# Kernel optimization log

Hardware: AMD Instinct MI355X
Metric: run time of the kernel (lower is better)

The kernel has to match this reference:

```python
import jax, jax.numpy as jnp
import numpy as np

D_MODEL = 1024
N_HEADS = 16
D_K = D_MODEL // N_HEADS
ROPE_THETA = 10000.0


def setup_inputs() -> dict:
    key = jax.random.key(0)
    ks = jax.random.split(key, 5)
    B, S = 2, 2048
    std = (2.0 / (D_MODEL + D_MODEL)) ** 0.5
    x = jax.random.normal(ks[0], (B, S, D_MODEL), dtype=jnp.float32)
    Wq = jax.random.normal(ks[1], (D_MODEL, D_MODEL), dtype=jnp.float32) * std
    Wk = jax.random.normal(ks[2], (D_MODEL, D_MODEL), dtype=jnp.float32) * std
    Wv = jax.random.normal(ks[3], (D_MODEL, D_MODEL), dtype=jnp.float32) * std
    Wo = jax.random.normal(ks[4], (D_MODEL, D_MODEL), dtype=jnp.float32) * std
    token_positions = jnp.arange(S, dtype=jnp.int64 if jax.config.jax_enable_x64 else jnp.int32)
    return {"x": x, "Wq": Wq, "Wk": Wk, "Wv": Wv, "Wo": Wo,
            "token_positions": token_positions}


def _apply_rope(t, token_positions):
    # t: [B, H, S, d_k]; token_positions: [S]
    inv_freq = 1.0 / (ROPE_THETA ** (jnp.arange(0, D_K, 2, dtype=jnp.float32) / D_K))  # [d_k/2]
    freqs = token_positions.astype(jnp.float32)[:, None] * inv_freq[None, :]  # [S, d_k/2]
    cos, sin = jnp.cos(freqs), jnp.sin(freqs)
    x1, x2 = t[..., ::2], t[..., 1::2]
    xr = x1 * cos - x2 * sin
    yr = x1 * sin + x2 * cos
    # interleave back to even/odd positions
    out = jnp.stack([xr, yr], axis=-1).reshape(t.shape)
    return out


def reference(x, Wq, Wk, Wv, Wo, token_positions):
    B, S, D = x.shape
    H, dk = N_HEADS, D_K
    # projections: weight is [d_out, d_in], applied as x @ W.T
    def proj_heads(W):
        y = jnp.einsum('bsd,ed->bse', x, W)
        return y.reshape(B, S, H, dk).transpose(0, 2, 1, 3)  # [B,H,S,dk]
    q = proj_heads(Wq)
    k = proj_heads(Wk)
    v = proj_heads(Wv)
    q = _apply_rope(q, token_positions)
    k = _apply_rope(k, token_positions)
    scores = jnp.einsum('bhqd,bhkd->bhqk', q, k) / jnp.sqrt(jnp.float32(dk))
    causal = jnp.tril(jnp.ones((S, S), dtype=bool))
    scores = jnp.where(causal, scores, -jnp.inf)
    attn = jax.nn.softmax(scores, axis=-1)
    out = jnp.einsum('bhqk,bhkd->bhqd', attn, v)  # [B,H,S,dk]
    out = out.transpose(0, 2, 1, 3).reshape(B, S, D)
    return jnp.einsum('bsd,ed->bse', out, Wo)
```

## Files before the change

### kernel.cpp

```cpp
#include <hip/hip_runtime.h>

typedef __bf16 bf16x8 __attribute__((ext_vector_type(8)));
typedef float f32x4 __attribute__((ext_vector_type(4)));
typedef unsigned short u16x8 __attribute__((ext_vector_type(8)));


__device__ __forceinline__ unsigned short f2bf(float f) {
  unsigned u = __builtin_bit_cast(unsigned, f);
  u = (u + 0x7FFFu + ((u >> 16) & 1u)) >> 16;
  return (unsigned short)u;
}

__device__ __forceinline__ unsigned cvt_pk_bf16(float lo, float hi) {
  unsigned r;
  asm("v_cvt_pk_bf16_f32 %0, %1, %2" : "=v"(r) : "v"(lo), "v"(hi));
  return r;
}

__device__ __forceinline__ void load_lds16(const void* g, void* l) {
  __builtin_amdgcn_global_load_lds(
      (__attribute__((address_space(1))) void*)g,
      (__attribute__((address_space(3))) void*)l, 16, 0, 0);
}

__global__ __launch_bounds__(256) void k_convert(
    const float* __restrict__ x,
    const float* __restrict__ wq, const float* __restrict__ wk,
    const float* __restrict__ wv, const float* __restrict__ wo,
    unsigned short* __restrict__ xb,
    unsigned short* __restrict__ wqb, unsigned short* __restrict__ wkb,
    unsigned short* __restrict__ wvb, unsigned short* __restrict__ wob) {
  const int g = blockIdx.x * 256 + threadIdx.x;
  const float* src;
  unsigned short* dst;
  int off;
  if (g < (1 << 20)) {
    src = x; dst = xb; off = g;
  } else {
    const int q = g - (1 << 20);
    const int t = q >> 18;
    off = q & ((1 << 18) - 1);
    src = (t == 0) ? wq : (t == 1) ? wk : (t == 2) ? wv : wo;
    dst = (t == 0) ? wqb : (t == 1) ? wkb : (t == 2) ? wvb : wob;
  }
  const float4 v = ((const float4*)src)[off];
  ushort4 r;
  r.x = f2bf(v.x); r.y = f2bf(v.y); r.z = f2bf(v.z); r.w = f2bf(v.w);
  ((ushort4*)dst)[off] = r;
}

__global__ __launch_bounds__(256) void k_rope_tab(const int* __restrict__ tpos,
                                                  float* __restrict__ ct,
                                                  float* __restrict__ st) {
  const int idx = blockIdx.x * 256 + threadIdx.x;
  const int s = idx >> 5, i = idx & 31;
  const double p = (double)tpos[s];
  const double f = p * pow(10000.0, -(double)(2 * i) / 64.0);
  ct[idx] = (float)cos(f);
  st[idx] = (float)sin(f);
}

__device__ __forceinline__ void gemm_core_1024(
    const unsigned short* __restrict__ Ag,
    const unsigned short* __restrict__ Bg,
    unsigned short* As, unsigned short* Bs, f32x4 (&acc)[4][4], int tid) {
  const int lane = tid & 63;
  const int w = tid >> 6;
  const int wm = (w >> 1) * 64;
  const int wn = (w & 1) * 64;
  const int lr = lane & 15;
  const int lg8 = (lane >> 4) * 8;
  const int c0 = tid, c1 = 256 + tid;
  const int ar0 = c0 >> 2, ac0 = (c0 & 3) * 8;
  const int ar1 = c1 >> 2, ac1 = (c1 & 3) * 8;

  auto stage = [&](int buf, int kt) {
    unsigned short* Ab = As + buf * 4096;
    unsigned short* Bb = Bs + buf * 4096;
    load_lds16(Ag + ar0 * 1024 + kt + ac0, Ab + c0 * 8);
    load_lds16(Ag + ar1 * 1024 + kt + ac1, Ab + c1 * 8);
    load_lds16(Bg + ar0 * 1024 + kt + ac0, Bb + c0 * 8);
    load_lds16(Bg + ar1 * 1024 + kt + ac1, Bb + c1 * 8);
  };

  stage(0, 0);
  stage(1, 32);
  int cur = 0;
  for (int ki = 0; ki < 32; ++ki) {
    if (ki + 2 < 32) {
      int nb = cur + 2; if (nb >= 3) nb -= 3;
      stage(nb, (ki + 2) * 32);
      asm volatile("s_waitcnt vmcnt(8)" ::: "memory");
    } else if (ki + 1 < 32) {
      asm volatile("s_waitcnt vmcnt(4)" ::: "memory");
    } else {
      asm volatile("s_waitcnt vmcnt(0)" ::: "memory");
    }
    __builtin_amdgcn_s_barrier();
    const unsigned short* Ab = As + cur * 4096;
    const unsigned short* Bb = Bs + cur * 4096;
    bf16x8 af[4], bfv[4];
#pragma unroll
    for (int mi = 0; mi < 4; ++mi)
      af[mi] = *(const bf16x8*)(Ab + (wm + mi * 16 + lr) * 32 + lg8);
#pragma unroll
    for (int ni = 0; ni < 4; ++ni)
      bfv[ni] = *(const bf16x8*)(Bb + (wn + ni * 16 + lr) * 32 + lg8);
    __builtin_amdgcn_s_setprio(1);
#pragma unroll
    for (int mi = 0; mi < 4; ++mi)
#pragma unroll
      for (int ni = 0; ni < 4; ++ni)
        acc[mi][ni] = __builtin_amdgcn_mfma_f32_16x16x32_bf16(
            af[mi], bfv[ni], acc[mi][ni], 0, 0, 0);
    __builtin_amdgcn_s_setprio(0);
    __builtin_amdgcn_s_barrier();
    ++cur; if (cur == 3) cur = 0;
  }
}

__global__ __launch_bounds__(256) void k_proj(
    const unsigned short* __restrict__ Xb,
    const unsigned short* __restrict__ Wq, const unsigned short* __restrict__ Wk,
    const unsigned short* __restrict__ Wv,
    const float* __restrict__ ctab, const float* __restrict__ stab,
    unsigned short* __restrict__ Qo, unsigned short* __restrict__ Ko,
    unsigned short* __restrict__ Vo) {
  __shared__ __align__(16) unsigned short As[3 * 128 * 32];
  __shared__ __align__(16) unsigned short Bs[3 * 128 * 32];
  const int z = blockIdx.z;
  const unsigned short* Wsel = (z == 0) ? Wq : (z == 1) ? Wk : Wv;
  unsigned short* Out = (z == 0) ? Qo : (z == 1) ? Ko : Vo;
  const int tid = threadIdx.x;
  const int bm = blockIdx.x * 128, bn = blockIdx.y * 128;
  f32x4 acc[4][4] = {};
  gemm_core_1024(Xb + (size_t)bm * 1024, Wsel + (size_t)bn * 1024, As, Bs, acc, tid);

  const int lane = tid & 63, w = tid >> 6;
  const int wm = (w >> 1) * 64, wn = (w & 1) * 64;
  const int lr = lane & 15, lg = lane >> 4;

  if (z == 2) {
#pragma unroll
    for (int mi = 0; mi < 4; ++mi) {
      const int r0 = bm + wm + mi * 16 + lg * 4;
      const int s = r0 & 2047, b = r0 >> 11;
#pragma unroll
      for (int ni = 0; ni < 4; ++ni) {
        const int e = bn + wn + ni * 16 + lr;
        const int h = e >> 6, d = e & 63;
        ushort4 pk;
        pk.x = f2bf(acc[mi][ni][0]);
        pk.y = f2bf(acc[mi][ni][1]);
        pk.z = f2bf(acc[mi][ni][2]);
        pk.w = f2bf(acc[mi][ni][3]);
        *(ushort4*)&Out[((size_t)(b * 16 + h) * 64 + d) * 2048 + s] = pk;
      }
    }
    return;
  }

  const bool odd = lane & 1;
#pragma unroll
  for (int mi = 0; mi < 4; ++mi) {
#pragma unroll
    for (int ni = 0; ni < 4; ++ni) {
#pragma unroll
      for (int reg = 0; reg < 4; ++reg) {
        const int r = bm + wm + mi * 16 + lg * 4 + reg;
        const int e = bn + wn + ni * 16 + lr;
        float val = acc[mi][ni][reg];
        const float partner = __shfl_xor(val, 1);
        const int s = r & 2047, b = r >> 11;
        const int h = e >> 6, d = e & 63;
        const int i = d >> 1;
        const float c = ctab[s * 32 + i];
        const float sn = stab[s * 32 + i];
        const float outv = odd ? (val * c + partner * sn) : (val * c - partner * sn);
        Out[((size_t)(b * 16 + h) * 2048 + s) * 64 + d] = f2bf(outv);
      }
    }
  }
}

__global__ __launch_bounds__(64, 2) void k_attn(
    const unsigned short* __restrict__ Q, const unsigned short* __restrict__ K,
    const unsigned short* __restrict__ Vt, unsigned short* __restrict__ O) {
  __shared__ __align__(16) unsigned short Vs[2][64 * 64];
  __shared__ __align__(16) unsigned short Pl[16 * 68];
  const int L = blockIdx.x;
  const int bh = (L & 7) * 4 + ((L >> 3) & 3);
  const int p = L >> 5;
  const int qrowA = p * 16, qrowB = (127 - p) * 16;
  const int Ta = (qrowA + 79) >> 6;
  const int Tb = (qrowB + 79) >> 6;
  const int TT = Ta + Tb;
  const int lane = threadIdx.x & 63;
  const int lr = lane & 15, lg = lane >> 4;
  const unsigned short* Qg = Q + (size_t)bh * 2048 * 64;
  const unsigned short* Kg = K + (size_t)bh * 2048 * 64;
  const unsigned short* Vg = Vt + (size_t)bh * 64 * 2048;

  bf16x8 qfA[2], qfB[2];
#pragma unroll
  for (int h = 0; h < 2; ++h) {
    qfA[h] = *(const bf16x8*)(Qg + (qrowA + lr) * 64 + h * 32 + lg * 8);
    qfB[h] = *(const bf16x8*)(Qg + (qrowB + lr) * 64 + h * 32 + lg * 8);
  }

  u16x8 ouv;
#pragma unroll
  for (int j = 0; j < 8; ++j) ouv[j] = 0x3F80;
  const bf16x8 onesf = __builtin_bit_cast(bf16x8, ouv);

  f32x4 oA[4] = {}, oB[4] = {};
  float mA[4], lA[4], mB[4], lB[4];
#pragma unroll
  for (int r = 0; r < 4; ++r) {
    mA[r] = -__builtin_inff(); lA[r] = 0.f;
    mB[r] = -__builtin_inff(); lB[r] = 0.f;
  }

  const float SCL = 0.125f * 1.44269504088896f;

  const int kbase = lr * 64 + lg * 8;
  const int vbase = (lane >> 3) * 2048 + (((lane & 7) ^ (lane >> 3)) * 8);

  auto kvof = [&](int t) { return (t < Tb) ? t : t - Tb; };
  auto loadK = [&](bf16x8 (&kd)[4][2], int kv) {
    const unsigned short* base = Kg + (size_t)kv * 4096 + kbase;
#pragma unroll
    for (int nt = 0; nt < 4; ++nt)
#pragma unroll
      for (int h = 0; h < 2; ++h)
        kd[nt][h] = *(const bf16x8*)(base + nt * 1024 + h * 32);
  };
  auto issueV = [&](int buf, int kv) {
    const unsigned short* src = Vg + kv * 64 + vbase;
    unsigned short* dst = &Vs[buf][0] + lane * 8;
#pragma unroll
    for (int i0 = 0; i0 < 8; ++i0)
      load_lds16(src + i0 * 16384, dst + i0 * 512);
  };

  auto core = [&](bf16x8 (&kc)[4][2], int kv, int T, bf16x8 (&qf)[2],
                  float (&m)[4], float (&l)[4], f32x4 (&oacc)[4], int qrow,
                  int vbuf, bool more) {
    const int kv0 = kv * 64;
    f32x4 sacc[4];
    __builtin_amdgcn_s_setprio(1);
#pragma unroll
    for (int nt = 0; nt < 4; ++nt) {
      f32x4 z = {0.f, 0.f, 0.f, 0.f};
      z = __builtin_amdgcn_mfma_f32_16x16x32_bf16(qf[0], kc[nt][0], z, 0, 0, 0);
      sacc[nt] = __builtin_amdgcn_mfma_f32_16x16x32_bf16(qf[1], kc[nt][1], z, 0, 0, 0);
    }
    __builtin_amdgcn_s_setprio(0);

    const bool needmask = (kv == T - 1);
    float pm[4];
#pragma unroll
    for (int r = 0; r < 4; ++r) pm[r] = -__builtin_inff();
#pragma unroll
    for (int nt = 0; nt < 4; ++nt)
#pragma unroll
      for (int reg = 0; reg < 4; ++reg) {
        float sv = sacc[nt][reg];
        if (needmask) {
          const int kg = kv0 + nt * 16 + lr;
          const int qg = qrow + lg * 4 + reg;
          if (kg > qg) sv = -__builtin_inff();
        }
        sacc[nt][reg] = sv;
        pm[reg] = fmaxf(pm[reg], sv);
      }
#pragma unroll
    for (int off = 1; off < 16; off <<= 1)
#pragma unroll
      for (int reg = 0; reg < 4; ++reg)
        pm[reg] = fmaxf(pm[reg], __shfl_xor(pm[reg], off));

    float gm = -1.f;
#pragma unroll
    for (int reg = 0; reg < 4; ++reg) gm = fmaxf(gm, pm[reg] - m[reg]);
    float msc[4];
    if (__any(gm > 0.f)) {
#pragma unroll
      for (int reg = 0; reg < 4; ++reg) {
        const float mn = fmaxf(m[reg], pm[reg]);
        const float al = exp2f(SCL * (m[reg] - mn));
        m[reg] = mn;
        msc[reg] = SCL * mn;
        l[reg] *= al;
#pragma unroll
        for (int nt = 0; nt < 4; ++nt) oacc[nt][reg] *= al;
      }
    } else {
#pragma unroll
      for (int reg = 0; reg < 4; ++reg) msc[reg] = SCL * m[reg];
    }

#pragma unroll
    for (int nt = 0; nt < 4; ++nt) {
      const float p0 = exp2f(sacc[nt][0] * SCL - msc[0]);
      const float p1 = exp2f(sacc[nt][1] * SCL - msc[1]);
      const float p2 = exp2f(sacc[nt][2] * SCL - msc[2]);
      const float p3 = exp2f(sacc[nt][3] * SCL - msc[3]);
      const unsigned w01 = cvt_pk_bf16(p0, p1);
      const unsigned w23 = cvt_pk_bf16(p2, p3);
      unsigned short* base = Pl + (lg * 4) * 68 + nt * 16 + lr;
      base[0] = (unsigned short)w01;
      base[68] = (unsigned short)(w01 >> 16);
      base[136] = (unsigned short)w23;
      base[204] = (unsigned short)(w23 >> 16);
    }
    bf16x8 pa[2];
#pragma unroll
    for (int ks = 0; ks < 2; ++ks)
      pa[ks] = *(const bf16x8*)(Pl + lr * 68 + ks * 32 + lg * 8);

    if (more) asm volatile("s_waitcnt vmcnt(16)" ::: "memory");
    else      asm volatile("s_waitcnt vmcnt(0)" ::: "memory");

    const unsigned short* Vw = &Vs[vbuf][0];
    __builtin_amdgcn_s_setprio(1);
    {
      f32x4 z = {0.f, 0.f, 0.f, 0.f};
      z = __builtin_amdgcn_mfma_f32_16x16x32_bf16(pa[0], onesf, z, 0, 0, 0);
      z = __builtin_amdgcn_mfma_f32_16x16x32_bf16(pa[1], onesf, z, 0, 0, 0);
#pragma unroll
      for (int reg = 0; reg < 4; ++reg) l[reg] += z[reg];
    }
#pragma unroll
    for (int nt = 0; nt < 4; ++nt) {
      const int row = nt * 16 + lr;
      const bf16x8 vb0 = *(const bf16x8*)(Vw + row * 64 + ((lg ^ (row & 7)) * 8));
      const bf16x8 vb1 = *(const bf16x8*)(Vw + row * 64 + (((lg + 4) ^ (row & 7)) * 8));
      oacc[nt] = __builtin_amdgcn_mfma_f32_16x16x32_bf16(pa[0], vb0, oacc[nt], 0, 0, 0);
      oacc[nt] = __builtin_amdgcn_mfma_f32_16x16x32_bf16(pa[1], vb1, oacc[nt], 0, 0, 0);
    }
    __builtin_amdgcn_s_setprio(0);
  };

  bf16x8 kbufA[4][2], kbufB[4][2];
  loadK(kbufA, 0);
  issueV(0, 0);

  auto iter = [&](int t, bf16x8 (&kc)[4][2], bf16x8 (&kn)[4][2]) {
    const int nxt = t + 1;
    const bool more = (nxt < TT);
    if (more) {
      const int kvn = kvof(nxt);
      loadK(kn, kvn);
      issueV(nxt & 1, kvn);
    }
    if (t < Tb) core(kc, t, Tb, qfB, mB, lB, oB, qrowB, t & 1, more);
    else        core(kc, t - Tb, Ta, qfA, mA, lA, oA, qrowA, t & 1, more);
  };

  int t = 0;
  for (;;) {
    iter(t, kbufA, kbufB); ++t; if (t >= TT) break;
    iter(t, kbufB, kbufA); ++t; if (t >= TT) break;
  }

  const int b = bh >> 4, h = bh & 15;
#pragma unroll
  for (int reg = 0; reg < 4; ++reg) {
    const float invA = 1.0f / lA[reg];
    const float invB = 1.0f / lB[reg];
    const int sA = qrowA + lg * 4 + reg;
    const int sB = qrowB + lg * 4 + reg;
#pragma unroll
    for (int nt = 0; nt < 4; ++nt) {
      const int dv = nt * 16 + lr;
      O[((size_t)b * 2048 + sA) * 1024 + h * 64 + dv] = f2bf(oA[nt][reg] * invA);
      O[((size_t)b * 2048 + sB) * 1024 + h * 64 + dv] = f2bf(oB[nt][reg] * invB);
    }
  }
}

__global__ __launch_bounds__(256) void k_out(const unsigned short* __restrict__ Ab,
                                             const unsigned short* __restrict__ Wo,
                                             float* __restrict__ Out) {
  __shared__ __align__(16) unsigned short As[3 * 128 * 32];
  __shared__ __align__(16) unsigned short Bs[3 * 128 * 32];
  const int tid = threadIdx.x;
  const int bm = blockIdx.x * 128, bn = blockIdx.y * 128;
  f32x4 acc[4][4] = {};
  gemm_core_1024(Ab + (size_t)bm * 1024, Wo + (size_t)bn * 1024, As, Bs, acc, tid);
  const int lane = tid & 63, w = tid >> 6;
  const int wm = (w >> 1) * 64, wn = (w & 1) * 64;
  const int lr = lane & 15, lg = lane >> 4;
#pragma unroll
  for (int mi = 0; mi < 4; ++mi)
#pragma unroll
    for (int ni = 0; ni < 4; ++ni)
#pragma unroll
      for (int reg = 0; reg < 4; ++reg) {
        const int r = bm + wm + mi * 16 + lg * 4 + reg;
        const int e = bn + wn + ni * 16 + lr;
        Out[(size_t)r * 1024 + e] = acc[mi][ni][reg];
      }
}

extern "C" void kernel_launch(void* const* d_in, const int* in_sizes, int n_in,
                              void* d_out, int out_size, void* d_ws, size_t ws_size,
                              hipStream_t stream) {
  const float* x = (const float*)d_in[0];
  const float* Wq = (const float*)d_in[1];
  const float* Wk = (const float*)d_in[2];
  const float* Wv = (const float*)d_in[3];
  const float* Wo = (const float*)d_in[4];
  const int* tpos = (const int*)d_in[5];
  float* out = (float*)d_out;
  char* ws = (char*)d_ws;
  const size_t MB = 1024 * 1024;
  unsigned short* xb = (unsigned short*)(ws);
  unsigned short* wqb = (unsigned short*)(ws + 8 * MB);
  unsigned short* wkb = (unsigned short*)(ws + 10 * MB);
  unsigned short* wvb = (unsigned short*)(ws + 12 * MB);
  unsigned short* wob = (unsigned short*)(ws + 14 * MB);
  unsigned short* Qb = (unsigned short*)(ws + 16 * MB);
  unsigned short* Kb = (unsigned short*)(ws + 24 * MB);
  unsigned short* Vtb = (unsigned short*)(ws + 32 * MB);
  unsigned short* Ab = (unsigned short*)(ws + 40 * MB);
  float* ctab = (float*)(ws + 48 * MB);
  float* stab = (float*)(ws + 48 * MB + 256 * 1024);

  k_convert<<<dim3(8192), dim3(256), 0, stream>>>(x, Wq, Wk, Wv, Wo, xb, wqb, wkb,
                                                  wvb, wob);
  k_rope_tab<<<dim3(256), dim3(256), 0, stream>>>(tpos, ctab, stab);
  k_proj<<<dim3(32, 8, 3), dim3(256), 0, stream>>>(xb, wqb, wkb, wvb, ctab, stab,
                                                   Qb, Kb, Vtb);
  k_attn<<<dim3(2048), dim3(64), 0, stream>>>(Qb, Kb, Vtb, Ab);
  k_out<<<dim3(32, 8), dim3(256), 0, stream>>>(Ab, wob, out);
}
```

Baseline: 175.2 us.

## Share K/V tiles between paired query blocks and transpose MFMA operand layout

The attention kernel now iterates over the key/value tiles once and, for each tile, computes both query blocks (A and B) so K registers and V LDS tiles are loaded once and reused, instead of streaming the tiles separately for each block. The MFMA operands are swapped (K×Q, V×P) so each lane owns one query row. Row max and sum then need only two cross-lane shuffles, the ones-matrix MFMA for the row sum is replaced by a register reduction, and P and O are stored as packed 4-element vectors. This cuts global and LDS traffic for the A block but raises register pressure, and it adds an lgkmcnt wait plus a serial second softmax pass per iteration.

```diff
diff --git a/kernel.cpp b/kernel.cpp
--- a/kernel.cpp
+++ b/kernel.cpp
@@ -194,7 +194,6 @@
   const int qrowA = p * 16, qrowB = (127 - p) * 16;
   const int Ta = (qrowA + 79) >> 6;
   const int Tb = (qrowB + 79) >> 6;
-  const int TT = Ta + Tb;
   const int lane = threadIdx.x & 63;
   const int lr = lane & 15, lg = lane >> 4;
   const unsigned short* Qg = Q + (size_t)bh * 2048 * 64;
@@ -208,25 +207,15 @@
     qfB[h] = *(const bf16x8*)(Qg + (qrowB + lr) * 64 + h * 32 + lg * 8);
   }
 
-  u16x8 ouv;
-#pragma unroll
-  for (int j = 0; j < 8; ++j) ouv[j] = 0x3F80;
-  const bf16x8 onesf = __builtin_bit_cast(bf16x8, ouv);
-
   f32x4 oA[4] = {}, oB[4] = {};
-  float mA[4], lA[4], mB[4], lB[4];
-#pragma unroll
-  for (int r = 0; r < 4; ++r) {
-    mA[r] = -__builtin_inff(); lA[r] = 0.f;
-    mB[r] = -__builtin_inff(); lB[r] = 0.f;
-  }
+  float mA = -__builtin_inff(), lA = 0.f;
+  float mB = -__builtin_inff(), lB = 0.f;
 
   const float SCL = 0.125f * 1.44269504088896f;
 
   const int kbase = lr * 64 + lg * 8;
   const int vbase = (lane >> 3) * 2048 + (((lane & 7) ^ (lane >> 3)) * 8);
 
-  auto kvof = [&](int t) { return (t < Tb) ? t : t - Tb; };
   auto loadK = [&](bf16x8 (&kd)[4][2], int kv) {
     const unsigned short* base = Kg + (size_t)kv * 4096 + kbase;
 #pragma unroll
@@ -243,141 +232,138 @@
       load_lds16(src + i0 * 16384, dst + i0 * 512);
   };
 
-  auto core = [&](bf16x8 (&kc)[4][2], int kv, int T, bf16x8 (&qf)[2],
-                  float (&m)[4], float (&l)[4], f32x4 (&oacc)[4], int qrow,
-                  int vbuf, bool more) {
-    const int kv0 = kv * 64;
-    f32x4 sacc[4];
+  auto process = [&](f32x4 (&s)[4], float& m, float& l, f32x4 (&oacc)[4],
+                     int qrow, bool needmask, int kv) {
+    if (needmask) {
+      const int qg = qrow + lr;
+#pragma unroll
+      for (int nt = 0; nt < 4; ++nt)
+#pragma unroll
+        for (int reg = 0; reg < 4; ++reg) {
+          const int kg = kv * 64 + nt * 16 + lg * 4 + reg;
+          if (kg > qg) s[nt][reg] = -__builtin_inff();
+        }
+    }
+    float t0 = fmaxf(fmaxf(s[0][0], s[0][1]), fmaxf(s[0][2], s[0][3]));
+    float t1 = fmaxf(fmaxf(s[1][0], s[1][1]), fmaxf(s[1][2], s[1][3]));
+    float t2 = fmaxf(fmaxf(s[2][0], s[2][1]), fmaxf(s[2][2], s[2][3]));
+    float t3 = fmaxf(fmaxf(s[3][0], s[3][1]), fmaxf(s[3][2], s[3][3]));
+    float pm = fmaxf(fmaxf(t0, t1), fmaxf(t2, t3));
+    pm = fmaxf(pm, __shfl_xor(pm, 16));
+    pm = fmaxf(pm, __shfl_xor(pm, 32));
+    if (__any(pm > m)) {
+      const float mn = fmaxf(m, pm);
+      const float al = exp2f(SCL * (m - mn));
+      m = mn;
+      l *= al;
+#pragma unroll
+      for (int nt = 0; nt < 4; ++nt)
+#pragma unroll
+        for (int reg = 0; reg < 4; ++reg) oacc[nt][reg] *= al;
+    }
+    const float msc = SCL * m;
+    float rs = 0.f;
+    unsigned short* prow = Pl + lr * 68;
+#pragma unroll
+    for (int nt = 0; nt < 4; ++nt) {
+      const float p0 = exp2f(s[nt][0] * SCL - msc);
+      const float p1 = exp2f(s[nt][1] * SCL - msc);
+      const float p2 = exp2f(s[nt][2] * SCL - msc);
+      const float p3 = exp2f(s[nt][3] * SCL - msc);
+      rs += (p0 + p1) + (p2 + p3);
+      const unsigned w01 = cvt_pk_bf16(p0, p1);
+      const unsigned w23 = cvt_pk_bf16(p2, p3);
+      ushort4 pk;
+      pk.x = (unsigned short)w01; pk.y = (unsigned short)(w01 >> 16);
+      pk.z = (unsigned short)w23; pk.w = (unsigned short)(w23 >> 16);
+      *(ushort4*)(prow + nt * 16 + lg * 4) = pk;
+    }
+    rs += __shfl_xor(rs, 16);
+    rs += __shfl_xor(rs, 32);
+    l += rs;
+  };
+
+  bf16x8 kbufA[4][2], kbufB[4][2];
+  loadK(kbufA, 0);
+  issueV(0, 0);
+
+  auto iter = [&](int t, bf16x8 (&kc)[4][2], bf16x8 (&kn)[4][2]) {
+    const bool more = (t + 1 < Tb);
+    const bool actA = (t < Ta);
+    asm volatile("s_waitcnt lgkmcnt(0)" ::: "memory");
+    if (more) { loadK(kn, t + 1); issueV((t + 1) & 1, t + 1); }
+
+    f32x4 sB[4], sA[4];
     __builtin_amdgcn_s_setprio(1);
 #pragma unroll
     for (int nt = 0; nt < 4; ++nt) {
       f32x4 z = {0.f, 0.f, 0.f, 0.f};
-      z = __builtin_amdgcn_mfma_f32_16x16x32_bf16(qf[0], kc[nt][0], z, 0, 0, 0);
-      sacc[nt] = __builtin_amdgcn_mfma_f32_16x16x32_bf16(qf[1], kc[nt][1], z, 0, 0, 0);
-    }
+      z = __builtin_amdgcn_mfma_f32_16x16x32_bf16(kc[nt][0], qfB[0], z, 0, 0, 0);
+      sB[nt] = __builtin_amdgcn_mfma_f32_16x16x32_bf16(kc[nt][1], qfB[1], z, 0, 0, 0);
+    }
+    if (actA)
+#pragma unroll
+      for (int nt = 0; nt < 4; ++nt) {
+        f32x4 z = {0.f, 0.f, 0.f, 0.f};
+        z = __builtin_amdgcn_mfma_f32_16x16x32_bf16(kc[nt][0], qfA[0], z, 0, 0, 0);
+        sA[nt] = __builtin_amdgcn_mfma_f32_16x16x32_bf16(kc[nt][1], qfA[1], z, 0, 0, 0);
+      }
     __builtin_amdgcn_s_setprio(0);
 
-    const bool needmask = (kv == T - 1);
-    float pm[4];
-#pragma unroll
-    for (int r = 0; r < 4; ++r) pm[r] = -__builtin_inff();
-#pragma unroll
-    for (int nt = 0; nt < 4; ++nt)
-#pragma unroll
-      for (int reg = 0; reg < 4; ++reg) {
-        float sv = sacc[nt][reg];
-        if (needmask) {
-          const int kg = kv0 + nt * 16 + lr;
-          const int qg = qrow + lg * 4 + reg;
-          if (kg > qg) sv = -__builtin_inff();
-        }
-        sacc[nt][reg] = sv;
-        pm[reg] = fmaxf(pm[reg], sv);
-      }
-#pragma unroll
-    for (int off = 1; off < 16; off <<= 1)
-#pragma unroll
-      for (int reg = 0; reg < 4; ++reg)
-        pm[reg] = fmaxf(pm[reg], __shfl_xor(pm[reg], off));
-
-    float gm = -1.f;
-#pragma unroll
-    for (int reg = 0; reg < 4; ++reg) gm = fmaxf(gm, pm[reg] - m[reg]);
-    float msc[4];
-    if (__any(gm > 0.f)) {
-#pragma unroll
-      for (int reg = 0; reg < 4; ++reg) {
-        const float mn = fmaxf(m[reg], pm[reg]);
-        const float al = exp2f(SCL * (m[reg] - mn));
-        m[reg] = mn;
-        msc[reg] = SCL * mn;
-        l[reg] *= al;
-#pragma unroll
-        for (int nt = 0; nt < 4; ++nt) oacc[nt][reg] *= al;
-      }
-    } else {
-#pragma unroll
-      for (int reg = 0; reg < 4; ++reg) msc[reg] = SCL * m[reg];
-    }
-
-#pragma unroll
-    for (int nt = 0; nt < 4; ++nt) {
-      const float p0 = exp2f(sacc[nt][0] * SCL - msc[0]);
-      const float p1 = exp2f(sacc[nt][1] * SCL - msc[1]);
-      const float p2 = exp2f(sacc[nt][2] * SCL - msc[2]);
-      const float p3 = exp2f(sacc[nt][3] * SCL - msc[3]);
-      const unsigned w01 = cvt_pk_bf16(p0, p1);
-      const unsigned w23 = cvt_pk_bf16(p2, p3);
-      unsigned short* base = Pl + (lg * 4) * 68 + nt * 16 + lr;
-      base[0] = (unsigned short)w01;
-      base[68] = (unsigned short)(w01 >> 16);
-      base[136] = (unsigned short)w23;
-      base[204] = (unsigned short)(w23 >> 16);
-    }
-    bf16x8 pa[2];
+    process(sB, mB, lB, oB, qrowB, t == Tb - 1, t);
+    bf16x8 paB[2], paA[2];
 #pragma unroll
     for (int ks = 0; ks < 2; ++ks)
-      pa[ks] = *(const bf16x8*)(Pl + lr * 68 + ks * 32 + lg * 8);
+      paB[ks] = *(const bf16x8*)(Pl + lr * 68 + ks * 32 + lg * 8);
+    if (actA) {
+      process(sA, mA, lA, oA, qrowA, t == Ta - 1, t);
+#pragma unroll
+      for (int ks = 0; ks < 2; ++ks)
+        paA[ks] = *(const bf16x8*)(Pl + lr * 68 + ks * 32 + lg * 8);
+    }
 
     if (more) asm volatile("s_waitcnt vmcnt(16)" ::: "memory");
     else      asm volatile("s_waitcnt vmcnt(0)" ::: "memory");
 
-    const unsigned short* Vw = &Vs[vbuf][0];
+    const unsigned short* Vw = &Vs[t & 1][0];
     __builtin_amdgcn_s_setprio(1);
-    {
-      f32x4 z = {0.f, 0.f, 0.f, 0.f};
-      z = __builtin_amdgcn_mfma_f32_16x16x32_bf16(pa[0], onesf, z, 0, 0, 0);
-      z = __builtin_amdgcn_mfma_f32_16x16x32_bf16(pa[1], onesf, z, 0, 0, 0);
-#pragma unroll
-      for (int reg = 0; reg < 4; ++reg) l[reg] += z[reg];
-    }
 #pragma unroll
     for (int nt = 0; nt < 4; ++nt) {
       const int row = nt * 16 + lr;
       const bf16x8 vb0 = *(const bf16x8*)(Vw + row * 64 + ((lg ^ (row & 7)) * 8));
       const bf16x8 vb1 = *(const bf16x8*)(Vw + row * 64 + (((lg + 4) ^ (row & 7)) * 8));
-      oacc[nt] = __builtin_amdgcn_mfma_f32_16x16x32_bf16(pa[0], vb0, oacc[nt], 0, 0, 0);
-      oacc[nt] = __builtin_amdgcn_mfma_f32_16x16x32_bf16(pa[1], vb1, oacc[nt], 0, 0, 0);
+      oB[nt] = __builtin_amdgcn_mfma_f32_16x16x32_bf16(vb0, paB[0], oB[nt], 0, 0, 0);
+      oB[nt] = __builtin_amdgcn_mfma_f32_16x16x32_bf16(vb1, paB[1], oB[nt], 0, 0, 0);
+      if (actA) {
+        oA[nt] = __builtin_amdgcn_mfma_f32_16x16x32_bf16(vb0, paA[0], oA[nt], 0, 0, 0);
+        oA[nt] = __builtin_amdgcn_mfma_f32_16x16x32_bf16(vb1, paA[1], oA[nt], 0, 0, 0);
+      }
     }
     __builtin_amdgcn_s_setprio(0);
-  };
-
-  bf16x8 kbufA[4][2], kbufB[4][2];
-  loadK(kbufA, 0);
-  issueV(0, 0);
-
-  auto iter = [&](int t, bf16x8 (&kc)[4][2], bf16x8 (&kn)[4][2]) {
-    const int nxt = t + 1;
-    const bool more = (nxt < TT);
-    if (more) {
-      const int kvn = kvof(nxt);
-      loadK(kn, kvn);
-      issueV(nxt & 1, kvn);
-    }
-    if (t < Tb) core(kc, t, Tb, qfB, mB, lB, oB, qrowB, t & 1, more);
-    else        core(kc, t - Tb, Ta, qfA, mA, lA, oA, qrowA, t & 1, more);
   };
 
   int t = 0;
   for (;;) {
-    iter(t, kbufA, kbufB); ++t; if (t >= TT) break;
-    iter(t, kbufB, kbufA); ++t; if (t >= TT) break;
+    iter(t, kbufA, kbufB); ++t; if (t >= Tb) break;
+    iter(t, kbufB, kbufA); ++t; if (t >= Tb) break;
   }
 
   const int b = bh >> 4, h = bh & 15;
-#pragma unroll
-  for (int reg = 0; reg < 4; ++reg) {
-    const float invA = 1.0f / lA[reg];
-    const float invB = 1.0f / lB[reg];
-    const int sA = qrowA + lg * 4 + reg;
-    const int sB = qrowB + lg * 4 + reg;
+  auto wrO = [&](f32x4 (&oacc)[4], float l, int qrow) {
+    const float inv = 1.0f / l;
+    unsigned short* dst = &O[((size_t)b * 2048 + qrow + lr) * 1024 + h * 64];
 #pragma unroll
     for (int nt = 0; nt < 4; ++nt) {
-      const int dv = nt * 16 + lr;
-      O[((size_t)b * 2048 + sA) * 1024 + h * 64 + dv] = f2bf(oA[nt][reg] * invA);
-      O[((size_t)b * 2048 + sB) * 1024 + h * 64 + dv] = f2bf(oB[nt][reg] * invB);
-    }
-  }
+      const unsigned w01 = cvt_pk_bf16(oacc[nt][0] * inv, oacc[nt][1] * inv);
+      const unsigned w23 = cvt_pk_bf16(oacc[nt][2] * inv, oacc[nt][3] * inv);
+      ushort4 pk;
+      pk.x = (unsigned short)w01; pk.y = (unsigned short)(w01 >> 16);
+      pk.z = (unsigned short)w23; pk.w = (unsigned short)(w23 >> 16);
+      *(ushort4*)(dst + nt * 16 + lg * 4) = pk;
+    }
+  };
+  wrO(oA, lA, qrowA);
+  wrO(oB, lB, qrowB);
 }
 
 __global__ __launch_bounds__(256) void k_out(const unsigned short* __restrict__ Ab,
```

After: 156.2 us. -10.8%, faster.
